# Optimization experiments

Hardware: AMD Instinct MI355X
Metric: run time of the kernel (lower is better)

## Reference

```python
import jax, jax.numpy as jnp
import numpy as np

NUM_HEADS = 16


def setup_inputs() -> dict:
    key = jax.random.key(0)
    ks = jax.random.split(key, 7)
    E = 1024
    s = 0.02
    return {
        "x": jax.random.normal(ks[0], (2, 2048, E), dtype=jnp.float32),
        "Wq": jax.random.normal(ks[1], (E, E), dtype=jnp.float32) * s,
        "bq": jax.random.normal(ks[2], (E,), dtype=jnp.float32) * s,
        "Wk": jax.random.normal(ks[3], (E, E), dtype=jnp.float32) * s,
        "bk": jax.random.normal(ks[4], (E,), dtype=jnp.float32) * s,
        "Wv": jax.random.normal(ks[5], (E, E), dtype=jnp.float32) * s,
        "bv": jax.random.normal(ks[6], (E,), dtype=jnp.float32) * s,
    }


def reference(x, Wq, bq, Wk, bk, Wv, bv):
    b, s, e = x.shape
    h = NUM_HEADS
    d = e // h  # head_dim = 64
    # nn.Linear: y = x @ W^T + b
    q = x @ Wq.T + bq
    k = x @ Wk.T + bk
    v = x @ Wv.T + bv
    # Faithful reshape chain from the source: (b,s,e)->(b,s,h,d)->(-1,s,d)
    # (raw reshape, NO transpose, matching the original buggy layout)
    q = q.reshape(b, s, h, d).reshape(-1, s, d)
    k = k.reshape(b, s, h, d).reshape(-1, s, d)
    v = v.reshape(b, s, h, d).reshape(-1, s, d)
    # Scaled scores; note the source returns qk @ v (softmax result discarded)
    scale = 1.0 / np.sqrt(d).astype(np.float32)
    qk = jnp.einsum('bqd,bkd->bqk', q, k) * scale  # [b*h, s, s]
    out = jnp.einsum('bqk,bkd->bqd', qk, v)        # [b*h, s, d]
    return out
```

## Files before the change

kernel.cpp:

```cpp
#include <hip/hip_runtime.h>
#include <hip/hip_bf16.h>


#define E_DIM 1024
#define N_ROWS 4096

typedef __attribute__((ext_vector_type(8))) short bf16x8;
typedef __attribute__((ext_vector_type(4))) float f32x4;

#define QB_U 0
#define KB_U 4194304
#define VB_U 8388608
#define XB_U 12582912
#define WB_U 16777216
#define P_F  9961472

__device__ __forceinline__ unsigned short f2b(float f) {
    union { float f; unsigned int i; } c; c.f = f;
    unsigned int r = c.i + 0x7FFFu + ((c.i >> 16) & 1u);
    return (unsigned short)(r >> 16);
}

__device__ __forceinline__ uint4 pack8(const f32x4 a, const f32x4 b) {
    uint4 o;
    o.x = (unsigned)f2b(a[0]) | ((unsigned)f2b(a[1]) << 16);
    o.y = (unsigned)f2b(a[2]) | ((unsigned)f2b(a[3]) << 16);
    o.z = (unsigned)f2b(b[0]) | ((unsigned)f2b(b[1]) << 16);
    o.w = (unsigned)f2b(b[2]) | ((unsigned)f2b(b[3]) << 16);
    return o;
}

typedef __attribute__((address_space(1))) const void* gptr_t;
typedef __attribute__((address_space(3))) void* lptr_t;
__device__ __forceinline__ void gl_lds16(const void* g, void* l) {
    __builtin_amdgcn_global_load_lds((gptr_t)g, (lptr_t)l, 16, 0, 0);
}

__device__ __forceinline__ int sw_idx(int row, int r) {
    return row * 64 + (((((r) >> 3) & 7) ^ (row & 7)) << 3) + (r & 7);
}

__global__ __launch_bounds__(256) void cvt_bf16(
    const float* __restrict__ x,  const float* __restrict__ wq,
    const float* __restrict__ wk, const float* __restrict__ wv,
    unsigned short* __restrict__ dst0)
{
    const int seg = blockIdx.y;
    const float* __restrict__ src;
    unsigned short* __restrict__ dst;
    if (seg < 4) { src = x + (size_t)seg * 1048576; dst = dst0 + (size_t)seg * 1048576; }
    else {
        src = (seg == 4) ? wq : (seg == 5) ? wk : wv;
        dst = dst0 + 4194304 + (size_t)(seg - 4) * 1048576;
    }
    const int i = blockIdx.x * 256 + threadIdx.x;
    const float4 a = *(const float4*)(src + (size_t)i * 8);
    const float4 b = *(const float4*)(src + (size_t)i * 8 + 4);
    uint4 o;
    o.x = (unsigned)f2b(a.x) | ((unsigned)f2b(a.y) << 16);
    o.y = (unsigned)f2b(a.z) | ((unsigned)f2b(a.w) << 16);
    o.z = (unsigned)f2b(b.x) | ((unsigned)f2b(b.y) << 16);
    o.w = (unsigned)f2b(b.z) | ((unsigned)f2b(b.w) << 16);
    *(uint4*)(dst + (size_t)i * 8) = o;
}

__global__ __launch_bounds__(256, 3) void qkv_gemm_mfma(
    const unsigned short* __restrict__ Xb,
    const unsigned short* __restrict__ Wb,
    const float* __restrict__ bq, const float* __restrict__ bk,
    const float* __restrict__ bv,
    unsigned short* __restrict__ qkv)
{
    const int which = blockIdx.z;
    const unsigned short* __restrict__ W = Wb + (size_t)which * (1024 * 1024);
    const float* __restrict__ bias = (which == 0) ? bq : (which == 1) ? bk : bv;
    unsigned short* __restrict__ Y = qkv + (size_t)which * ((size_t)N_ROWS * E_DIM);

    __shared__ __align__(16) unsigned short Als[128 * 64];
    __shared__ __align__(16) unsigned short Bls[128 * 64];

    const int tid  = threadIdx.x;
    const int w    = tid >> 6;
    const int lane = tid & 63;
    const int m0 = blockIdx.x * 128;
    const int n0 = blockIdx.y * 128;
    const int wm = (w >> 1) * 64;
    const int wn = (w & 1) * 64;

    f32x4 acc[4][4];
    #pragma unroll
    for (int i = 0; i < 4; ++i)
        #pragma unroll
        for (int j = 0; j < 4; ++j)
            acc[i][j] = f32x4{0.f, 0.f, 0.f, 0.f};

    const int srow = lane >> 3;
    const int skc  = ((lane & 7) ^ (lane >> 3)) * 8;
    const int quad = lane >> 4;
    const int fm   = lane & 15;
    const int sw8  = fm & 7;

    for (int k0 = 0; k0 < E_DIM; k0 += 64) {
        #pragma unroll
        for (int c = 0; c < 4; ++c) {
            const int r = w * 32 + c * 8;
            gl_lds16((const void*)(Xb + (size_t)(m0 + r + srow) * E_DIM + k0 + skc),
                     (void*)((char*)Als + r * 128 + lane * 16));
            gl_lds16((const void*)(W + (size_t)(n0 + r + srow) * E_DIM + k0 + skc),
                     (void*)((char*)Bls + r * 128 + lane * 16));
        }
        __syncthreads();

        #pragma unroll
        for (int kk = 0; kk < 2; ++kk) {
            const int slot = ((kk * 4 + quad) ^ sw8) * 8;
            bf16x8 af[4], bf[4];
            #pragma unroll
            for (int t = 0; t < 4; ++t) {
                af[t] = *(const bf16x8*)(Als + (wm + t * 16 + fm) * 64 + slot);
                bf[t] = *(const bf16x8*)(Bls + (wn + t * 16 + fm) * 64 + slot);
            }
            #pragma unroll
            for (int rt = 0; rt < 4; ++rt)
                #pragma unroll
                for (int ct = 0; ct < 4; ++ct)
                    acc[rt][ct] = __builtin_amdgcn_mfma_f32_16x16x32_bf16(
                        af[rt], bf[ct], acc[rt][ct], 0, 0, 0);
        }
        __syncthreads();
    }

    float bcol[4];
    #pragma unroll
    for (int ct = 0; ct < 4; ++ct) bcol[ct] = bias[n0 + wn + ct * 16 + fm];

    const int rbase = (lane >> 4) * 4;
    #pragma unroll
    for (int rt = 0; rt < 4; ++rt) {
        #pragma unroll
        for (int ct = 0; ct < 4; ++ct) {
            #pragma unroll
            for (int r = 0; r < 4; ++r) {
                const int row = m0 + wm + rt * 16 + rbase + r;
                const int col = n0 + wn + ct * 16 + fm;
                Y[(size_t)row * E_DIM + col] = f2b(acc[rt][ct][r] + bcol[ct]);
            }
        }
    }
}

__global__ __launch_bounds__(256) void kT_mfma(
    const unsigned short* __restrict__ qkv, float* __restrict__ P)
{
    const size_t base = (size_t)blockIdx.x * (2048 * 64) + (size_t)blockIdx.y * (128 * 64);
    const unsigned short* __restrict__ Kb = qkv + KB_U + base;
    const unsigned short* __restrict__ Vb = qkv + VB_U + base;
    float* __restrict__ Pout = P + ((size_t)blockIdx.x * 16 + blockIdx.y) * 4096;

    __shared__ __align__(16) unsigned short Kt[64 * 64];
    __shared__ __align__(16) unsigned short Vt[64 * 64];

    const int tid  = threadIdx.x;
    const int w    = tid >> 6;
    const int lane = tid & 63;
    const int eo   = w * 16;
    const int quad = lane >> 4;
    const int fm   = lane & 15;
    const int sw8  = fm & 7;

    f32x4 acc[4];
    #pragma unroll
    for (int nt = 0; nt < 4; ++nt) acc[nt] = f32x4{0.f, 0.f, 0.f, 0.f};

    for (int rb = 0; rb < 128; rb += 64) {
        union { uint4 u; unsigned short s[8]; } k0, k1, v0, v1;
        const size_t ga = (size_t)(rb + lane) * 64 + eo;
        k0.u = *(const uint4*)(Kb + ga);
        k1.u = *(const uint4*)(Kb + ga + 8);
        v0.u = *(const uint4*)(Vb + ga);
        v1.u = *(const uint4*)(Vb + ga + 8);
        __syncthreads();
        #pragma unroll
        for (int j = 0; j < 8; ++j) {
            Kt[sw_idx(eo + j, lane)]     = k0.s[j];
            Kt[sw_idx(eo + 8 + j, lane)] = k1.s[j];
            Vt[sw_idx(eo + j, lane)]     = v0.s[j];
            Vt[sw_idx(eo + 8 + j, lane)] = v1.s[j];
        }
        __syncthreads();
        #pragma unroll
        for (int kk = 0; kk < 2; ++kk) {
            const int slot = ((kk * 4 + quad) ^ sw8) << 3;
            const bf16x8 af = *(const bf16x8*)(Vt + (w * 16 + fm) * 64 + slot);
            #pragma unroll
            for (int nt = 0; nt < 4; ++nt) {
                const bf16x8 bf = *(const bf16x8*)(Kt + (nt * 16 + fm) * 64 + slot);
                acc[nt] = __builtin_amdgcn_mfma_f32_16x16x32_bf16(af, bf, acc[nt], 0, 0, 0);
            }
        }
    }

    const int rbase = (lane >> 4) * 4;
    #pragma unroll
    for (int nt = 0; nt < 4; ++nt)
        #pragma unroll
        for (int r = 0; r < 4; ++r)
            Pout[(size_t)(w * 16 + rbase + r) * 64 + nt * 16 + fm] = acc[nt][r];
}

__global__ __launch_bounds__(256, 2) void qT_fused(
    const unsigned short* __restrict__ qkv,
    const float* __restrict__ P,
    float* __restrict__ out)
{
    __shared__ __align__(16) unsigned short Als[128 * 64];
    __shared__ __align__(16) unsigned short Tls[64 * 64];

    const int b    = blockIdx.x;
    const int i    = (b & 7) + ((b >> 3) & 3) * 8;
    const int sub  = b >> 5;
    const int r0   = (i * 16 + sub) * 128;
    const int tid  = threadIdx.x;
    const int w    = tid >> 6;
    const int lane = tid & 63;
    const int quad = lane >> 4;
    const int fm   = lane & 15;
    const int sw8  = fm & 7;

    const unsigned short* __restrict__ Qb = qkv + QB_U + (size_t)r0 * 64;

    const int soff = (lane >> 3) * 64 + (((lane & 7) ^ (lane >> 3)) << 3);
    #pragma unroll
    for (int c = 0; c < 4; ++c)
        gl_lds16((const void*)(Qb + (w * 4 + c) * 512 + soff),
                 (void*)((char*)Als + (w * 4 + c) * 1024));

    {
        const int d  = tid >> 2;
        const int e0 = (tid & 3) << 4;
        const float* p = P + (size_t)i * 65536 + (size_t)d * 64 + e0;
        f32x4 s0{0.f,0.f,0.f,0.f}, s1{0.f,0.f,0.f,0.f};
        f32x4 s2{0.f,0.f,0.f,0.f}, s3{0.f,0.f,0.f,0.f};
        #pragma unroll
        for (int c = 0; c < 16; ++c) {
            s0 += *(const f32x4*)(p + (size_t)c * 4096);
            s1 += *(const f32x4*)(p + (size_t)c * 4096 + 4);
            s2 += *(const f32x4*)(p + (size_t)c * 4096 + 8);
            s3 += *(const f32x4*)(p + (size_t)c * 4096 + 12);
        }
        const int c0 = e0 >> 3;
        *(uint4*)(Tls + d * 64 + ((c0 ^ (d & 7)) << 3))       = pack8(s0, s1);
        *(uint4*)(Tls + d * 64 + (((c0 + 1) ^ (d & 7)) << 3)) = pack8(s2, s3);
    }
    __syncthreads();

    bf16x8 af[2][2], bf[4][2];
    #pragma unroll
    for (int mt = 0; mt < 2; ++mt)
        #pragma unroll
        for (int kk = 0; kk < 2; ++kk)
            af[mt][kk] = *(const bf16x8*)(Als + (w * 32 + mt * 16 + fm) * 64
                                          + (((kk * 4 + quad) ^ sw8) << 3));
    #pragma unroll
    for (int nt = 0; nt < 4; ++nt)
        #pragma unroll
        for (int kk = 0; kk < 2; ++kk)
            bf[nt][kk] = *(const bf16x8*)(Tls + (nt * 16 + fm) * 64
                                          + (((kk * 4 + quad) ^ sw8) << 3));

    f32x4 acc[2][4];
    #pragma unroll
    for (int mt = 0; mt < 2; ++mt)
        #pragma unroll
        for (int nt = 0; nt < 4; ++nt)
            acc[mt][nt] = f32x4{0.f, 0.f, 0.f, 0.f};

    #pragma unroll
    for (int kk = 0; kk < 2; ++kk)
        #pragma unroll
        for (int mt = 0; mt < 2; ++mt)
            #pragma unroll
            for (int nt = 0; nt < 4; ++nt)
                acc[mt][nt] = __builtin_amdgcn_mfma_f32_16x16x32_bf16(
                    af[mt][kk], bf[nt][kk], acc[mt][nt], 0, 0, 0);

    const int rbase = (lane >> 4) * 4;
    #pragma unroll
    for (int mt = 0; mt < 2; ++mt) {
        #pragma unroll
        for (int nt = 0; nt < 4; ++nt) {
            #pragma unroll
            for (int r = 0; r < 4; ++r) {
                const int row = r0 + w * 32 + mt * 16 + rbase + r;
                const int col = nt * 16 + fm;
                out[(size_t)row * 64 + col] = 0.125f * acc[mt][nt][r];
            }
        }
    }
}

extern "C" void kernel_launch(void* const* d_in, const int* in_sizes, int n_in,
                              void* d_out, int out_size, void* d_ws, size_t ws_size,
                              hipStream_t stream)
{
    const float* x  = (const float*)d_in[0];
    const float* Wq = (const float*)d_in[1];
    const float* bq = (const float*)d_in[2];
    const float* Wk = (const float*)d_in[3];
    const float* bk = (const float*)d_in[4];
    const float* Wv = (const float*)d_in[5];
    const float* bv = (const float*)d_in[6];
    float* wsf = (float*)d_ws;
    unsigned short* wsu = (unsigned short*)d_ws;
    float* out = (float*)d_out;

    dim3 gCvt(512, 7);
    cvt_bf16<<<gCvt, 256, 0, stream>>>(x, Wq, Wk, Wv, wsu + XB_U);

    dim3 gA(N_ROWS / 128, E_DIM / 128, 3);
    qkv_gemm_mfma<<<gA, 256, 0, stream>>>(wsu + XB_U, wsu + WB_U,
                                          bq, bk, bv, wsu);

    dim3 gB(32, 16);
    kT_mfma<<<gB, 256, 0, stream>>>(wsu, wsf + P_F);

    qT_fused<<<512, 256, 0, stream>>>(wsu, wsf + P_F, out);
}
```

Baseline: 132.3 us.

## Fuse K/V projection with K^T V reduction in one GEMM kernel

Merges the QKV projection and the K^T·V partial-product kernel. Blocks with z=1 compute Q as before. Blocks with z=0 compute both the K and V tiles for the same rows and columns, then stage them transposed in shared memory and compute the 64x64 K^T V partials directly. This avoids writing K and V to global memory, reading them back, and one kernel launch. The cost is that each K/V block runs two GEMM loops serially, which gives uneven work across blocks (Q blocks do half as much) and fewer blocks in the grid.

```diff
diff --git a/kernel.cpp b/kernel.cpp
--- a/kernel.cpp
+++ b/kernel.cpp
@@ -9,8 +9,6 @@
 typedef __attribute__((ext_vector_type(4))) float f32x4;
 
 #define QB_U 0
-#define KB_U 4194304
-#define VB_U 8388608
 #define XB_U 12582912
 #define WB_U 16777216
 #define P_F  9961472
@@ -38,6 +36,10 @@
 
 __device__ __forceinline__ int sw_idx(int row, int r) {
     return row * 64 + (((((r) >> 3) & 7) ^ (row & 7)) << 3) + (r & 7);
+}
+
+__device__ __forceinline__ int sw128(int row, int r) {
+    return row * 128 + ((((r >> 3) ^ (row & 7)) & 15) << 3) + (r & 7);
 }
 
 __global__ __launch_bounds__(256) void cvt_bf16(
@@ -64,41 +66,18 @@
     *(uint4*)(dst + (size_t)i * 8) = o;
 }
 
-__global__ __launch_bounds__(256, 3) void qkv_gemm_mfma(
-    const unsigned short* __restrict__ Xb,
-    const unsigned short* __restrict__ Wb,
-    const float* __restrict__ bq, const float* __restrict__ bk,
-    const float* __restrict__ bv,
-    unsigned short* __restrict__ qkv)
-{
-    const int which = blockIdx.z;
-    const unsigned short* __restrict__ W = Wb + (size_t)which * (1024 * 1024);
-    const float* __restrict__ bias = (which == 0) ? bq : (which == 1) ? bk : bv;
-    unsigned short* __restrict__ Y = qkv + (size_t)which * ((size_t)N_ROWS * E_DIM);
-
-    __shared__ __align__(16) unsigned short Als[128 * 64];
-    __shared__ __align__(16) unsigned short Bls[128 * 64];
-
-    const int tid  = threadIdx.x;
-    const int w    = tid >> 6;
-    const int lane = tid & 63;
-    const int m0 = blockIdx.x * 128;
-    const int n0 = blockIdx.y * 128;
-    const int wm = (w >> 1) * 64;
-    const int wn = (w & 1) * 64;
-
-    f32x4 acc[4][4];
-    #pragma unroll
-    for (int i = 0; i < 4; ++i)
-        #pragma unroll
-        for (int j = 0; j < 4; ++j)
-            acc[i][j] = f32x4{0.f, 0.f, 0.f, 0.f};
-
-    const int srow = lane >> 3;
-    const int skc  = ((lane & 7) ^ (lane >> 3)) * 8;
+__device__ __forceinline__ void gemm_loop(
+    const unsigned short* __restrict__ Xb, const unsigned short* __restrict__ W,
+    unsigned short* Als, unsigned short* Bls,
+    int m0, int n0, int w, int lane, f32x4 (&acc)[4][4])
+{
     const int quad = lane >> 4;
     const int fm   = lane & 15;
     const int sw8  = fm & 7;
+    const int srow = lane >> 3;
+    const int skc  = ((lane & 7) ^ (lane >> 3)) * 8;
+    const int wm = (w >> 1) * 64;
+    const int wn = (w & 1) * 64;
 
     for (int k0 = 0; k0 < E_DIM; k0 += 64) {
         #pragma unroll
@@ -129,83 +108,136 @@
         }
         __syncthreads();
     }
-
-    float bcol[4];
-    #pragma unroll
-    for (int ct = 0; ct < 4; ++ct) bcol[ct] = bias[n0 + wn + ct * 16 + fm];
-
-    const int rbase = (lane >> 4) * 4;
-    #pragma unroll
-    for (int rt = 0; rt < 4; ++rt) {
-        #pragma unroll
-        for (int ct = 0; ct < 4; ++ct) {
-            #pragma unroll
-            for (int r = 0; r < 4; ++r) {
-                const int row = m0 + wm + rt * 16 + rbase + r;
-                const int col = n0 + wn + ct * 16 + fm;
-                Y[(size_t)row * E_DIM + col] = f2b(acc[rt][ct][r] + bcol[ct]);
-            }
-        }
-    }
-}
-
-__global__ __launch_bounds__(256) void kT_mfma(
-    const unsigned short* __restrict__ qkv, float* __restrict__ P)
-{
-    const size_t base = (size_t)blockIdx.x * (2048 * 64) + (size_t)blockIdx.y * (128 * 64);
-    const unsigned short* __restrict__ Kb = qkv + KB_U + base;
-    const unsigned short* __restrict__ Vb = qkv + VB_U + base;
-    float* __restrict__ Pout = P + ((size_t)blockIdx.x * 16 + blockIdx.y) * 4096;
-
-    __shared__ __align__(16) unsigned short Kt[64 * 64];
-    __shared__ __align__(16) unsigned short Vt[64 * 64];
+}
+
+__global__ __launch_bounds__(256, 3) void qkv_kt_fused(
+    const unsigned short* __restrict__ Xb,
+    const unsigned short* __restrict__ Wb,
+    const float* __restrict__ bq, const float* __restrict__ bk,
+    const float* __restrict__ bv,
+    unsigned short* __restrict__ qkv,
+    float* __restrict__ P)
+{
+    __shared__ __align__(16) unsigned short S[16384];
 
     const int tid  = threadIdx.x;
     const int w    = tid >> 6;
     const int lane = tid & 63;
-    const int eo   = w * 16;
     const int quad = lane >> 4;
     const int fm   = lane & 15;
     const int sw8  = fm & 7;
-
-    f32x4 acc[4];
-    #pragma unroll
-    for (int nt = 0; nt < 4; ++nt) acc[nt] = f32x4{0.f, 0.f, 0.f, 0.f};
-
-    for (int rb = 0; rb < 128; rb += 64) {
-        union { uint4 u; unsigned short s[8]; } k0, k1, v0, v1;
-        const size_t ga = (size_t)(rb + lane) * 64 + eo;
-        k0.u = *(const uint4*)(Kb + ga);
-        k1.u = *(const uint4*)(Kb + ga + 8);
-        v0.u = *(const uint4*)(Vb + ga);
-        v1.u = *(const uint4*)(Vb + ga + 8);
+    const int rbase = quad * 4;
+    const int m0 = blockIdx.x * 128;
+    const int n0 = blockIdx.y * 128;
+    const int wm = (w >> 1) * 64;
+    const int wn = (w & 1) * 64;
+
+    f32x4 acc[4][4];
+    #pragma unroll
+    for (int i = 0; i < 4; ++i)
+        #pragma unroll
+        for (int j = 0; j < 4; ++j)
+            acc[i][j] = f32x4{0.f, 0.f, 0.f, 0.f};
+
+    if (blockIdx.z == 1) {
+        gemm_loop(Xb, Wb, S, S + 8192, m0, n0, w, lane, acc);
+
+        float bcol[4];
+        #pragma unroll
+        for (int ct = 0; ct < 4; ++ct) bcol[ct] = bq[n0 + wn + ct * 16 + fm];
+
+        #pragma unroll
+        for (int rt = 0; rt < 4; ++rt) {
+            #pragma unroll
+            for (int ct = 0; ct < 4; ++ct) {
+                #pragma unroll
+                for (int r = 0; r < 4; ++r) {
+                    const int row = m0 + wm + rt * 16 + rbase + r;
+                    const int col = n0 + wn + ct * 16 + fm;
+                    qkv[(size_t)row * E_DIM + col] = f2b(acc[rt][ct][r] + bcol[ct]);
+                }
+            }
+        }
+        return;
+    }
+
+    gemm_loop(Xb, Wb + 1048576, S, S + 8192, m0, n0, w, lane, acc);
+
+    float bcK[4];
+    #pragma unroll
+    for (int ct = 0; ct < 4; ++ct) bcK[ct] = bk[n0 + wn + ct * 16 + fm];
+
+    uint2 pk[4][4];
+    #pragma unroll
+    for (int rt = 0; rt < 4; ++rt)
+        #pragma unroll
+        for (int ct = 0; ct < 4; ++ct) {
+            uint2 v;
+            v.x = (unsigned)f2b(acc[rt][ct][0] + bcK[ct])
+                | ((unsigned)f2b(acc[rt][ct][1] + bcK[ct]) << 16);
+            v.y = (unsigned)f2b(acc[rt][ct][2] + bcK[ct])
+                | ((unsigned)f2b(acc[rt][ct][3] + bcK[ct]) << 16);
+            pk[rt][ct] = v;
+        }
+
+    #pragma unroll
+    for (int i = 0; i < 4; ++i)
+        #pragma unroll
+        for (int j = 0; j < 4; ++j)
+            acc[i][j] = f32x4{0.f, 0.f, 0.f, 0.f};
+    gemm_loop(Xb, Wb + 2097152, S, S + 8192, m0, n0, w, lane, acc);
+
+    float bcV[4];
+    #pragma unroll
+    for (int ct = 0; ct < 4; ++ct) bcV[ct] = bv[n0 + wn + ct * 16 + fm];
+
+    unsigned short* Kt = S;
+    unsigned short* Vt = S + 8192;
+
+    #pragma unroll
+    for (int h = 0; h < 2; ++h) {
         __syncthreads();
-        #pragma unroll
-        for (int j = 0; j < 8; ++j) {
-            Kt[sw_idx(eo + j, lane)]     = k0.s[j];
-            Kt[sw_idx(eo + 8 + j, lane)] = k1.s[j];
-            Vt[sw_idx(eo + j, lane)]     = v0.s[j];
-            Vt[sw_idx(eo + 8 + j, lane)] = v1.s[j];
+        if ((w & 1) == h) {
+            #pragma unroll
+            for (int rt = 0; rt < 4; ++rt)
+                #pragma unroll
+                for (int ct = 0; ct < 4; ++ct) {
+                    const int e  = ct * 16 + fm;
+                    const int r0 = wm + rt * 16 + rbase;
+                    *(uint2*)(Kt + sw128(e, r0)) = pk[rt][ct];
+                    uint2 pv;
+                    pv.x = (unsigned)f2b(acc[rt][ct][0] + bcV[ct])
+                         | ((unsigned)f2b(acc[rt][ct][1] + bcV[ct]) << 16);
+                    pv.y = (unsigned)f2b(acc[rt][ct][2] + bcV[ct])
+                         | ((unsigned)f2b(acc[rt][ct][3] + bcV[ct]) << 16);
+                    *(uint2*)(Vt + sw128(e, r0)) = pv;
+                }
         }
         __syncthreads();
-        #pragma unroll
-        for (int kk = 0; kk < 2; ++kk) {
+
+        f32x4 t[4];
+        #pragma unroll
+        for (int nt = 0; nt < 4; ++nt) t[nt] = f32x4{0.f, 0.f, 0.f, 0.f};
+        #pragma unroll
+        for (int kk = 0; kk < 4; ++kk) {
             const int slot = ((kk * 4 + quad) ^ sw8) << 3;
-            const bf16x8 af = *(const bf16x8*)(Vt + (w * 16 + fm) * 64 + slot);
+            const bf16x8 af = *(const bf16x8*)(Vt + (w * 16 + fm) * 128 + slot);
             #pragma unroll
             for (int nt = 0; nt < 4; ++nt) {
-                const bf16x8 bf = *(const bf16x8*)(Kt + (nt * 16 + fm) * 64 + slot);
-                acc[nt] = __builtin_amdgcn_mfma_f32_16x16x32_bf16(af, bf, acc[nt], 0, 0, 0);
+                const bf16x8 bf = *(const bf16x8*)(Kt + (nt * 16 + fm) * 128 + slot);
+                t[nt] = __builtin_amdgcn_mfma_f32_16x16x32_bf16(af, bf, t[nt], 0, 0, 0);
             }
         }
-    }
-
-    const int rbase = (lane >> 4) * 4;
-    #pragma unroll
-    for (int nt = 0; nt < 4; ++nt)
-        #pragma unroll
-        for (int r = 0; r < 4; ++r)
-            Pout[(size_t)(w * 16 + rbase + r) * 64 + nt * 16 + fm] = acc[nt][r];
+
+        const int ih    = blockIdx.x;
+        const int chunk = blockIdx.y * 2 + h;
+        float* __restrict__ Pout = P + ((size_t)ih * 16 + chunk) * 4096;
+        #pragma unroll
+        for (int nt = 0; nt < 4; ++nt)
+            #pragma unroll
+            for (int r = 0; r < 4; ++r)
+                Pout[(size_t)(w * 16 + rbase + r) * 64 + nt * 16 + fm] = t[nt][r];
+    }
 }
 
 __global__ __launch_bounds__(256, 2) void qT_fused(
@@ -317,12 +349,9 @@
     dim3 gCvt(512, 7);
     cvt_bf16<<<gCvt, 256, 0, stream>>>(x, Wq, Wk, Wv, wsu + XB_U);
 
-    dim3 gA(N_ROWS / 128, E_DIM / 128, 3);
-    qkv_gemm_mfma<<<gA, 256, 0, stream>>>(wsu + XB_U, wsu + WB_U,
-                                          bq, bk, bv, wsu);
-
-    dim3 gB(32, 16);
-    kT_mfma<<<gB, 256, 0, stream>>>(wsu, wsf + P_F);
+    dim3 gG(N_ROWS / 128, E_DIM / 128, 2);
+    qkv_kt_fused<<<gG, 256, 0, stream>>>(wsu + XB_U, wsu + WB_U,
+                                         bq, bk, bv, wsu, wsf + P_F);
 
     qT_fused<<<512, 256, 0, stream>>>(wsu, wsf + P_F, out);
 }
```

Result: slower. 140.7 us (+6.3%).
